# Kernel optimization log

Hardware: AMD Instinct MI355X
Metric: run time of the kernel (lower is better)

## Reference

```python
import jax, jax.numpy as jnp
import numpy as np

B, SQ, SK, D, H = 8, 2048, 2048, 512, 8
QP, KP, VP = 512, 512, 4096  # VP must equal D*H for O_w to accept the concat


def setup_inputs() -> dict:
    key = jax.random.key(0)
    ks = jax.random.split(key, 9)
    q_in = jax.random.normal(ks[0], (B, SQ, D), dtype=jnp.float32)
    k_in = jax.random.normal(ks[1], (B, SK, D), dtype=jnp.float32)
    v_in = jax.random.normal(ks[2], (B, SK, D), dtype=jnp.float32)
    mask = jax.random.randint(ks[3], (B, SQ, SK), 0, 2, dtype=jnp.int32)
    W_q = jax.random.normal(ks[4], (D, QP), dtype=jnp.float32) * 0.02
    W_k = jax.random.normal(ks[5], (D, KP), dtype=jnp.float32) * 0.02
    W_v = jax.random.normal(ks[6], (D, VP), dtype=jnp.float32) * 0.02
    W_o = jax.random.normal(ks[7], (VP, D), dtype=jnp.float32) * 0.02
    b_o = jnp.zeros((D,), dtype=jnp.float32)
    return {"q_in": q_in, "k_in": k_in, "v_in": v_in,
            "W_q": W_q, "W_k": W_k, "W_v": W_v, "W_o": W_o, "b_o": b_o,
            "mask": mask}


def reference(q_in, k_in, v_in, W_q, W_k, W_v, W_o, b_o, mask):
    b, sq, d = q_in.shape
    sk = k_in.shape[1]
    # NOTE: original scales by sqrt(input_dim // num_heads), NOT actual head dim
    scale = jnp.asarray(np.sqrt(d // H), dtype=q_in.dtype)
    q = q_in @ W_q  # (B, Sq, QP)
    k = k_in @ W_k  # (B, Sk, KP)
    v = v_in @ W_v  # (B, Sk, VP)
    q_h = q.reshape(b, sq, H, -1).transpose(0, 2, 1, 3)  # (B,H,Sq,dq)
    k_h = k.reshape(b, sk, H, -1).transpose(0, 2, 1, 3)  # (B,H,Sk,dk)
    v_h = v.reshape(b, sk, H, -1).transpose(0, 2, 1, 3)  # (B,H,Sk,dv)
    attn = jnp.einsum('bhid,bhkd->bhik', q_h, k_h)  # (B,H,Sq,Sk)
    attn = jnp.where(mask[:, None, :, :] == 0, jnp.asarray(-1e9, attn.dtype), attn)
    attn = jax.nn.softmax(attn / scale, axis=-1)
    out = attn @ v_h  # (B,H,Sq,dv)
    # Faithful to original bug: transpose(0,1) swaps BATCH and HEAD, then reshape
    out = jnp.transpose(out, (1, 0, 2, 3)).reshape(b, sq, -1)  # (B,Sq,H*dv)
    return out @ W_o + b_o
```

## Files before the change

### kernel.cpp

```cpp
#include <hip/hip_runtime.h>
#include <math.h>

typedef __bf16 bf16x8 __attribute__((ext_vector_type(8)));
typedef float fx4 __attribute__((ext_vector_type(4)));
typedef unsigned short u16;
typedef unsigned short u16x8 __attribute__((ext_vector_type(8)));
typedef unsigned int u32;
typedef unsigned char u8;

__device__ __forceinline__ fx4 mfma16(bf16x8 a, bf16x8 b, fx4 c) {
  return __builtin_amdgcn_mfma_f32_16x16x32_bf16(a, b, c, 0, 0, 0);
}
__device__ __forceinline__ u16 f2bf(float f) {
  u32 u = __float_as_uint(f);
  u += 0x7fffu + ((u >> 16) & 1u);
  return (u16)(u >> 16);
}
__device__ __forceinline__ float ex2(float x) { return __builtin_amdgcn_exp2f(x); }

#define BB 8
#define SS 2048
#define DD 512
#define HH 8
#define DQ 64
#define DV 512
#define VP 4096

#define OFF_QP  ((size_t)0)
#define OFF_KP  ((size_t)16777216)
#define OFF_WQT ((size_t)33554432)
#define OFF_WKT ((size_t)34078720)
#define OFF_WVT ((size_t)34603008)
#define OFF_WOT ((size_t)38797312)
#define OFF_MB  ((size_t)42991616)
#define OFF_VT  ((size_t)76546048)
#define OFF_XB  ((size_t)210763776)

__global__ __launch_bounds__(256) void transpose_w(const float* __restrict__ W,
                                                   u16* __restrict__ Wt,
                                                   int K, int N) {
  __shared__ float t[32][33];
  const int n0 = blockIdx.x * 32, k0 = blockIdx.y * 32;
  const int tx = threadIdx.x & 31, ty = threadIdx.x >> 5;
#pragma unroll
  for (int i = 0; i < 32; i += 8)
    t[ty + i][tx] = W[(size_t)(k0 + ty + i) * N + n0 + tx];
  __syncthreads();
#pragma unroll
  for (int i = 0; i < 32; i += 8)
    Wt[(size_t)(n0 + ty + i) * K + k0 + tx] = f2bf(t[tx][ty + i]);
}

__global__ __launch_bounds__(256) void mask_pack(const int* __restrict__ m,
                                                 u8* __restrict__ mb) {
  const size_t i = ((size_t)blockIdx.x * 256 + threadIdx.x) * 16;
  int4 a0 = *(const int4*)(m + i);
  int4 a1 = *(const int4*)(m + i + 4);
  int4 a2 = *(const int4*)(m + i + 8);
  int4 a3 = *(const int4*)(m + i + 12);
  uint4 o;
  o.x = (a0.x ? 1u : 0u) | ((a0.y ? 1u : 0u) << 8) | ((a0.z ? 1u : 0u) << 16) | ((a0.w ? 1u : 0u) << 24);
  o.y = (a1.x ? 1u : 0u) | ((a1.y ? 1u : 0u) << 8) | ((a1.z ? 1u : 0u) << 16) | ((a1.w ? 1u : 0u) << 24);
  o.z = (a2.x ? 1u : 0u) | ((a2.y ? 1u : 0u) << 8) | ((a2.z ? 1u : 0u) << 16) | ((a2.w ? 1u : 0u) << 24);
  o.w = (a3.x ? 1u : 0u) | ((a3.y ? 1u : 0u) << 8) | ((a3.z ? 1u : 0u) << 16) | ((a3.w ? 1u : 0u) << 24);
  *(uint4*)(mb + i) = o;
}

template <int AFP32, int EPI>
__global__ __launch_bounds__(256) void gemm_bt(const void* __restrict__ Ap,
                                               const u16* __restrict__ Bt,
                                               void* __restrict__ Cp,
                                               int M, int N, int K,
                                               const float* __restrict__ bias,
                                               float scale) {
  __shared__ union {
    struct { u16 As[128 * 32]; u16 Bs[128 * 32]; } s;
    u16 T[4][64 * 68];
  } sm;
  const int tid = threadIdx.x;
  const int lane = tid & 63, w = tid >> 6;
  const int lhi = lane >> 4, llo = lane & 15;
  const int wm = w >> 1, wn = w & 1;
  const int m0 = blockIdx.y * 128, n0 = blockIdx.x * 128;

  fx4 acc[4][4];
#pragma unroll
  for (int i = 0; i < 4; ++i)
#pragma unroll
    for (int j = 0; j < 4; ++j) acc[i][j] = (fx4){0.f, 0.f, 0.f, 0.f};

  for (int k0 = 0; k0 < K; k0 += 32) {
    if (AFP32) {
      const float* A = (const float*)Ap;
      const int row = tid >> 1, co = (tid & 1) * 16;
      const float* src = A + (size_t)(m0 + row) * K + k0 + co;
      float4 v0 = *(const float4*)(src + 0);
      float4 v1 = *(const float4*)(src + 4);
      float4 v2 = *(const float4*)(src + 8);
      float4 v3 = *(const float4*)(src + 12);
      u16x8 p0 = {f2bf(v0.x), f2bf(v0.y), f2bf(v0.z), f2bf(v0.w),
                  f2bf(v1.x), f2bf(v1.y), f2bf(v1.z), f2bf(v1.w)};
      u16x8 p1 = {f2bf(v2.x), f2bf(v2.y), f2bf(v2.z), f2bf(v2.w),
                  f2bf(v3.x), f2bf(v3.y), f2bf(v3.z), f2bf(v3.w)};
      *(u16x8*)&sm.s.As[row * 32 + co] = p0;
      *(u16x8*)&sm.s.As[row * 32 + co + 8] = p1;
    } else {
      const u16* A = (const u16*)Ap;
#pragma unroll
      for (int j = 0; j < 2; ++j) {
        int cc = j * 256 + tid;
        int row = cc >> 2, c8 = (cc & 3) * 8;
        *(uint4*)&sm.s.As[cc * 8] = *(const uint4*)&A[(size_t)(m0 + row) * K + k0 + c8];
      }
    }
#pragma unroll
    for (int j = 0; j < 2; ++j) {
      int cc = j * 256 + tid;
      int row = cc >> 2, c8 = (cc & 3) * 8;
      *(uint4*)&sm.s.Bs[cc * 8] = *(const uint4*)&Bt[(size_t)(n0 + row) * K + k0 + c8];
    }
    __syncthreads();
    bf16x8 af[4], bfv[4];
#pragma unroll
    for (int mi = 0; mi < 4; ++mi)
      af[mi] = *(const bf16x8*)&sm.s.As[(wm * 64 + mi * 16 + llo) * 32 + lhi * 8];
#pragma unroll
    for (int ni = 0; ni < 4; ++ni)
      bfv[ni] = *(const bf16x8*)&sm.s.Bs[(wn * 64 + ni * 16 + llo) * 32 + lhi * 8];
#pragma unroll
    for (int mi = 0; mi < 4; ++mi)
#pragma unroll
      for (int ni = 0; ni < 4; ++ni)
        acc[mi][ni] = mfma16(af[mi], bfv[ni], acc[mi][ni]);
    __syncthreads();
  }

  const int rbase = m0 + wm * 64, cbase = n0 + wn * 64;
  if (EPI == 0) {
    u16* C = (u16*)Cp;
#pragma unroll
    for (int mi = 0; mi < 4; ++mi) {
      int r0 = rbase + mi * 16 + lhi * 4;
#pragma unroll
      for (int ni = 0; ni < 4; ++ni) {
        int c = cbase + ni * 16 + llo;
#pragma unroll
        for (int r = 0; r < 4; ++r)
          C[(size_t)(r0 + r) * N + c] = f2bf(acc[mi][ni][r] * scale);
      }
    }
  } else if (EPI == 1) {
    u16* Tw = &sm.T[w][0];
#pragma unroll
    for (int mi = 0; mi < 4; ++mi)
#pragma unroll
      for (int ni = 0; ni < 4; ++ni) {
        ushort4 pk;
        pk.x = f2bf(acc[mi][ni][0]);
        pk.y = f2bf(acc[mi][ni][1]);
        pk.z = f2bf(acc[mi][ni][2]);
        pk.w = f2bf(acc[mi][ni][3]);
        *(ushort4*)&Tw[(ni * 16 + llo) * 68 + mi * 16 + lhi * 4] = pk;
      }
    u16* VtC = (u16*)Cp;
    const int bsel = rbase >> 11;
    const int sb = rbase & 2047;
    u16* dst = VtC + ((size_t)(bsel * VP + cbase + lane)) * SS + sb;
#pragma unroll
    for (int j = 0; j < 8; ++j) {
      u16x8 vv = *(u16x8*)&Tw[lane * 68 + j * 8];
      *(u16x8*)&dst[j * 8] = vv;
    }
  } else {
    float* C = (float*)Cp;
#pragma unroll
    for (int ni = 0; ni < 4; ++ni) {
      int c = cbase + ni * 16 + llo;
      float bv = bias[c];
#pragma unroll
      for (int mi = 0; mi < 4; ++mi) {
        int r0 = rbase + mi * 16 + lhi * 4;
#pragma unroll
        for (int r = 0; r < 4; ++r)
          C[(size_t)(r0 + r) * N + c] = acc[mi][ni][r] + bv;
      }
    }
  }
}

#define KB 128
#define SMS 132
__global__ __launch_bounds__(256, 2) void attn(const u16* __restrict__ Qp,
                                               const u16* __restrict__ Kp,
                                               const u16* __restrict__ Vt,
                                               const u8* __restrict__ mb,
                                               u16* __restrict__ Xb) {
  const int lin = blockIdx.x;
  const int xcd = lin & 7, idx = lin >> 3;
  const int chunk = idx >> 5, qt = idx & 31;
  const int b = chunk >> 1, dvh = chunk & 1, h = xcd;
  const int m0 = qt * 64;
  const int tid = threadIdx.x, w = tid >> 6, lane = tid & 63;
  const int lhi = lane >> 4, llo = lane & 15;

  __shared__ float Ssm[64 * SMS];
  __shared__ u16 Psm[64 * SMS];
  __shared__ float sm_l[64];

  bf16x8 qf[4][2];
#pragma unroll
  for (int mt = 0; mt < 4; ++mt)
#pragma unroll
    for (int ks = 0; ks < 2; ++ks)
      qf[mt][ks] = *(const bf16x8*)&Qp[(size_t)(b * SS + m0 + mt * 16 + llo) * 512 +
                                       h * DQ + ks * 32 + lhi * 8];

  fx4 acc[4][4];
#pragma unroll
  for (int mt = 0; mt < 4; ++mt)
#pragma unroll
    for (int nt = 0; nt < 4; ++nt) acc[mt][nt] = (fx4){0.f, 0.f, 0.f, 0.f};

  const int r8 = tid >> 3, c16 = (tid & 7) * 16;
  const u8* mr0 = mb + (size_t)(b * SS + m0 + r8) * SS;
  const u8* mr1 = mr0 + 32 * SS;
  float ls0 = 0.f, ls1 = 0.f;

  const int cw = w * 32;
  const size_t kbase = (size_t)(b * SS) * 512 + h * DQ + lhi * 8;
  const size_t vbase =
      (size_t)(b * VP + h * DV + dvh * 256 + w * 64 + llo) * SS + lhi * 8;

  for (int n0 = 0; n0 < SS; n0 += KB) {
    bf16x8 kf[2][2];
#pragma unroll
    for (int ct = 0; ct < 2; ++ct)
#pragma unroll
      for (int ks = 0; ks < 2; ++ks)
        kf[ct][ks] = *(const bf16x8*)&Kp[kbase +
                                         (size_t)(n0 + cw + ct * 16 + llo) * 512 +
                                         ks * 32];
    uint4 ma0 = *(const uint4*)&mr0[n0 + c16];
    uint4 ma1 = *(const uint4*)&mr1[n0 + c16];

#pragma unroll
    for (int ct = 0; ct < 2; ++ct)
#pragma unroll
      for (int mt = 0; mt < 4; ++mt) {
        fx4 s = (fx4){0.f, 0.f, 0.f, 0.f};
        s = mfma16(qf[mt][0], kf[ct][0], s);
        s = mfma16(qf[mt][1], kf[ct][1], s);
#pragma unroll
        for (int r = 0; r < 4; ++r)
          Ssm[(mt * 16 + lhi * 4 + r) * SMS + cw + ct * 16 + llo] = s[r];
      }
    __syncthreads();

#pragma unroll
    for (int half = 0; half < 2; ++half) {
      const int rr = r8 + half * 32;
      const uint4 mv = half ? ma1 : ma0;
      const float* Sr = &Ssm[rr * SMS + c16];
      float4 xa = *(const float4*)(Sr + 0);
      float4 xb = *(const float4*)(Sr + 4);
      float4 xc = *(const float4*)(Sr + 8);
      float4 xd = *(const float4*)(Sr + 12);
      const float NEG = -1.0e9f;
      float p0 = ex2((mv.x & 0x000000ffu) ? xa.x : NEG);
      float p1 = ex2((mv.x & 0x0000ff00u) ? xa.y : NEG);
      float p2 = ex2((mv.x & 0x00ff0000u) ? xa.z : NEG);
      float p3 = ex2((mv.x & 0xff000000u) ? xa.w : NEG);
      float p4 = ex2((mv.y & 0x000000ffu) ? xb.x : NEG);
      float p5 = ex2((mv.y & 0x0000ff00u) ? xb.y : NEG);
      float p6 = ex2((mv.y & 0x00ff0000u) ? xb.z : NEG);
      float p7 = ex2((mv.y & 0xff000000u) ? xb.w : NEG);
      float p8 = ex2((mv.z & 0x000000ffu) ? xc.x : NEG);
      float p9 = ex2((mv.z & 0x0000ff00u) ? xc.y : NEG);
      float p10 = ex2((mv.z & 0x00ff0000u) ? xc.z : NEG);
      float p11 = ex2((mv.z & 0xff000000u) ? xc.w : NEG);
      float p12 = ex2((mv.w & 0x000000ffu) ? xd.x : NEG);
      float p13 = ex2((mv.w & 0x0000ff00u) ? xd.y : NEG);
      float p14 = ex2((mv.w & 0x00ff0000u) ? xd.z : NEG);
      float p15 = ex2((mv.w & 0xff000000u) ? xd.w : NEG);
      u16x8 qa = {f2bf(p0), f2bf(p1), f2bf(p2), f2bf(p3),
                  f2bf(p4), f2bf(p5), f2bf(p6), f2bf(p7)};
      u16x8 qb = {f2bf(p8), f2bf(p9), f2bf(p10), f2bf(p11),
                  f2bf(p12), f2bf(p13), f2bf(p14), f2bf(p15)};
      *(u16x8*)&Psm[rr * SMS + c16] = qa;
      *(u16x8*)&Psm[rr * SMS + c16 + 8] = qb;
      float ps = (((p0 + p1) + (p2 + p3)) + ((p4 + p5) + (p6 + p7))) +
                 (((p8 + p9) + (p10 + p11)) + ((p12 + p13) + (p14 + p15)));
      if (half) ls1 += ps; else ls0 += ps;
    }
    __syncthreads();

#pragma unroll
    for (int kk = 0; kk < 4; ++kk) {
      bf16x8 pf[4];
#pragma unroll
      for (int mt = 0; mt < 4; ++mt)
        pf[mt] = *(const bf16x8*)&Psm[(mt * 16 + llo) * SMS + kk * 32 + lhi * 8];
      __builtin_amdgcn_s_setprio(1);
#pragma unroll
      for (int nt = 0; nt < 4; ++nt) {
        bf16x8 vf = *(const bf16x8*)&Vt[vbase + (size_t)(nt * 16) * SS + n0 + kk * 32];
#pragma unroll
        for (int mt = 0; mt < 4; ++mt)
          acc[mt][nt] = mfma16(pf[mt], vf, acc[mt][nt]);
      }
      __builtin_amdgcn_s_setprio(0);
    }
  }

  ls0 += __shfl_xor(ls0, 1); ls0 += __shfl_xor(ls0, 2); ls0 += __shfl_xor(ls0, 4);
  ls1 += __shfl_xor(ls1, 1); ls1 += __shfl_xor(ls1, 2); ls1 += __shfl_xor(ls1, 4);
  if ((tid & 7) == 0) { sm_l[r8] = ls0; sm_l[r8 + 32] = ls1; }
  __syncthreads();

  float linv[4][4];
#pragma unroll
  for (int mt = 0; mt < 4; ++mt)
#pragma unroll
    for (int r = 0; r < 4; ++r) linv[mt][r] = 1.0f / sm_l[mt * 16 + lhi * 4 + r];

  u16* Xs = (u16*)Ssm;
  const int er = tid >> 4, ec = (tid & 15) * 16;
#pragma unroll
  for (int mt = 0; mt < 4; ++mt) {
#pragma unroll
    for (int nt = 0; nt < 4; ++nt)
#pragma unroll
      for (int r = 0; r < 4; ++r)
        Xs[(lhi * 4 + r) * 264 + w * 64 + nt * 16 + llo] =
            f2bf(acc[mt][nt][r] * linv[mt][r]);
    __syncthreads();
    {
      const u16* src = Xs + er * 264 + ec;
      u16* dst = Xb + (size_t)((h * 8 + b) * SS + m0 + mt * 16 + er) * 512 +
                 dvh * 256 + ec;
      uint4 a0 = *(const uint4*)(src + 0);
      uint4 a1 = *(const uint4*)(src + 8);
      *(uint4*)(dst + 0) = a0;
      *(uint4*)(dst + 8) = a1;
    }
    __syncthreads();
  }
}

extern "C" void kernel_launch(void* const* d_in, const int* in_sizes, int n_in,
                              void* d_out, int out_size, void* d_ws, size_t ws_size,
                              hipStream_t stream) {
  (void)in_sizes; (void)n_in; (void)out_size; (void)ws_size;
  const float* q_in = (const float*)d_in[0];
  const float* k_in = (const float*)d_in[1];
  const float* v_in = (const float*)d_in[2];
  const float* W_q  = (const float*)d_in[3];
  const float* W_k  = (const float*)d_in[4];
  const float* W_v  = (const float*)d_in[5];
  const float* W_o  = (const float*)d_in[6];
  const float* b_o  = (const float*)d_in[7];
  const int*   mask = (const int*)d_in[8];

  char* ws = (char*)d_ws;
  u16* Qp   = (u16*)(ws + OFF_QP);
  u16* Kp   = (u16*)(ws + OFF_KP);
  u16* Wqt  = (u16*)(ws + OFF_WQT);
  u16* Wkt  = (u16*)(ws + OFF_WKT);
  u16* Wvt  = (u16*)(ws + OFF_WVT);
  u16* Wot  = (u16*)(ws + OFF_WOT);
  u8*  Mb   = (u8*)(ws + OFF_MB);
  u16* Vt   = (u16*)(ws + OFF_VT);
  u16* Xb   = (u16*)(ws + OFF_XB);

  transpose_w<<<dim3(16, 16), 256, 0, stream>>>(W_q, Wqt, 512, 512);
  transpose_w<<<dim3(16, 16), 256, 0, stream>>>(W_k, Wkt, 512, 512);
  transpose_w<<<dim3(128, 16), 256, 0, stream>>>(W_v, Wvt, 512, 4096);
  transpose_w<<<dim3(16, 128), 256, 0, stream>>>(W_o, Wot, 4096, 512);
  mask_pack<<<dim3(8192), 256, 0, stream>>>(mask, Mb);

  gemm_bt<1, 0><<<dim3(4, 128), 256, 0, stream>>>(q_in, Wqt, Qp, 16384, 512, 512, nullptr, 0.18033688011112f);
  gemm_bt<1, 0><<<dim3(4, 128), 256, 0, stream>>>(k_in, Wkt, Kp, 16384, 512, 512, nullptr, 1.0f);
  gemm_bt<1, 1><<<dim3(32, 128), 256, 0, stream>>>(v_in, Wvt, Vt, 16384, 4096, 512, nullptr, 1.0f);

  attn<<<dim3(4096), 256, 0, stream>>>(Qp, Kp, Vt, Mb, Xb);

  gemm_bt<0, 2><<<dim3(4, 128), 256, 0, stream>>>(Xb, Wot, d_out, 16384, 512, 4096, b_o, 1.0f);
}
```

Before: 1.392 ms.

## Fuse softmax into QK MFMA registers with swizzled double-buffered P tile

After: 1.492 ms (median of 2 runs). +7.2%, slower.

```diff
diff --git a/kernel.cpp b/kernel.cpp
--- a/kernel.cpp
+++ b/kernel.cpp
@@ -15,6 +15,10 @@
   u32 u = __float_as_uint(f);
   u += 0x7fffu + ((u >> 16) & 1u);
   return (u16)(u >> 16);
+}
+__device__ __forceinline__ u16 bfc(float f) {
+  __bf16 h = (__bf16)f;
+  return __builtin_bit_cast(u16, h);
 }
 __device__ __forceinline__ float ex2(float x) { return __builtin_amdgcn_exp2f(x); }
 
@@ -189,8 +193,7 @@
 }
 
 #define KB 128
-#define SMS 132
-__global__ __launch_bounds__(256, 2) void attn(const u16* __restrict__ Qp,
+__global__ __launch_bounds__(256, 3) void attn(const u16* __restrict__ Qp,
                                                const u16* __restrict__ Kp,
                                                const u16* __restrict__ Vt,
                                                const u8* __restrict__ mb,
@@ -202,9 +205,10 @@
   const int m0 = qt * 64;
   const int tid = threadIdx.x, w = tid >> 6, lane = tid & 63;
   const int lhi = lane >> 4, llo = lane & 15;
-
-  __shared__ float Ssm[64 * SMS];
-  __shared__ u16 Psm[64 * SMS];
+  const int xork = (llo & 7) << 4;
+
+  __shared__ u16 Psm[2][64 * 128];
+  __shared__ float sm_lw[4][64];
   __shared__ float sm_l[64];
 
   bf16x8 qf[4][2];
@@ -220,77 +224,53 @@
   for (int mt = 0; mt < 4; ++mt)
 #pragma unroll
     for (int nt = 0; nt < 4; ++nt) acc[mt][nt] = (fx4){0.f, 0.f, 0.f, 0.f};
-
-  const int r8 = tid >> 3, c16 = (tid & 7) * 16;
-  const u8* mr0 = mb + (size_t)(b * SS + m0 + r8) * SS;
-  const u8* mr1 = mr0 + 32 * SS;
-  float ls0 = 0.f, ls1 = 0.f;
-
-  const int cw = w * 32;
+  float lp[4] = {0.f, 0.f, 0.f, 0.f};
+
   const size_t kbase = (size_t)(b * SS) * 512 + h * DQ + lhi * 8;
   const size_t vbase =
       (size_t)(b * VP + h * DV + dvh * 256 + w * 64 + llo) * SS + lhi * 8;
+  const u8* mrow[4];
+#pragma unroll
+  for (int mt = 0; mt < 4; ++mt)
+    mrow[mt] = mb + (size_t)(b * SS + m0 + mt * 16 + llo) * SS + w * 32 + lhi * 4;
 
   for (int n0 = 0; n0 < SS; n0 += KB) {
+    const int buf = (n0 >> 7) & 1;
+    char* Pb = (char*)&Psm[buf][0];
+
     bf16x8 kf[2][2];
 #pragma unroll
-    for (int ct = 0; ct < 2; ++ct)
+    for (int st = 0; st < 2; ++st)
 #pragma unroll
       for (int ks = 0; ks < 2; ++ks)
-        kf[ct][ks] = *(const bf16x8*)&Kp[kbase +
-                                         (size_t)(n0 + cw + ct * 16 + llo) * 512 +
+        kf[st][ks] = *(const bf16x8*)&Kp[kbase +
+                                         (size_t)(n0 + w * 32 + st * 16 + llo) * 512 +
                                          ks * 32];
-    uint4 ma0 = *(const uint4*)&mr0[n0 + c16];
-    uint4 ma1 = *(const uint4*)&mr1[n0 + c16];
-
-#pragma unroll
-    for (int ct = 0; ct < 2; ++ct)
-#pragma unroll
-      for (int mt = 0; mt < 4; ++mt) {
+    u32 mv[4][2];
+#pragma unroll
+    for (int mt = 0; mt < 4; ++mt)
+#pragma unroll
+      for (int st = 0; st < 2; ++st)
+        mv[mt][st] = *(const u32*)(mrow[mt] + n0 + st * 16);
+
+#pragma unroll
+    for (int mt = 0; mt < 4; ++mt) {
+      const int qL = mt * 16 + llo;
+      char* prow = Pb + qL * 256;
+#pragma unroll
+      for (int st = 0; st < 2; ++st) {
         fx4 s = (fx4){0.f, 0.f, 0.f, 0.f};
-        s = mfma16(qf[mt][0], kf[ct][0], s);
-        s = mfma16(qf[mt][1], kf[ct][1], s);
-#pragma unroll
-        for (int r = 0; r < 4; ++r)
-          Ssm[(mt * 16 + lhi * 4 + r) * SMS + cw + ct * 16 + llo] = s[r];
-      }
-    __syncthreads();
-
-#pragma unroll
-    for (int half = 0; half < 2; ++half) {
-      const int rr = r8 + half * 32;
-      const uint4 mv = half ? ma1 : ma0;
-      const float* Sr = &Ssm[rr * SMS + c16];
-      float4 xa = *(const float4*)(Sr + 0);
-      float4 xb = *(const float4*)(Sr + 4);
-      float4 xc = *(const float4*)(Sr + 8);
-      float4 xd = *(const float4*)(Sr + 12);
-      const float NEG = -1.0e9f;
-      float p0 = ex2((mv.x & 0x000000ffu) ? xa.x : NEG);
-      float p1 = ex2((mv.x & 0x0000ff00u) ? xa.y : NEG);
-      float p2 = ex2((mv.x & 0x00ff0000u) ? xa.z : NEG);
-      float p3 = ex2((mv.x & 0xff000000u) ? xa.w : NEG);
-      float p4 = ex2((mv.y & 0x000000ffu) ? xb.x : NEG);
-      float p5 = ex2((mv.y & 0x0000ff00u) ? xb.y : NEG);
-      float p6 = ex2((mv.y & 0x00ff0000u) ? xb.z : NEG);
-      float p7 = ex2((mv.y & 0xff000000u) ? xb.w : NEG);
-      float p8 = ex2((mv.z & 0x000000ffu) ? xc.x : NEG);
-      float p9 = ex2((mv.z & 0x0000ff00u) ? xc.y : NEG);
-      float p10 = ex2((mv.z & 0x00ff0000u) ? xc.z : NEG);
-      float p11 = ex2((mv.z & 0xff000000u) ? xc.w : NEG);
-      float p12 = ex2((mv.w & 0x000000ffu) ? xd.x : NEG);
-      float p13 = ex2((mv.w & 0x0000ff00u) ? xd.y : NEG);
-      float p14 = ex2((mv.w & 0x00ff0000u) ? xd.z : NEG);
-      float p15 = ex2((mv.w & 0xff000000u) ? xd.w : NEG);
-      u16x8 qa = {f2bf(p0), f2bf(p1), f2bf(p2), f2bf(p3),
-                  f2bf(p4), f2bf(p5), f2bf(p6), f2bf(p7)};
-      u16x8 qb = {f2bf(p8), f2bf(p9), f2bf(p10), f2bf(p11),
-                  f2bf(p12), f2bf(p13), f2bf(p14), f2bf(p15)};
-      *(u16x8*)&Psm[rr * SMS + c16] = qa;
-      *(u16x8*)&Psm[rr * SMS + c16 + 8] = qb;
-      float ps = (((p0 + p1) + (p2 + p3)) + ((p4 + p5) + (p6 + p7))) +
-                 (((p8 + p9) + (p10 + p11)) + ((p12 + p13) + (p14 + p15)));
-      if (half) ls1 += ps; else ls0 += ps;
+        s = mfma16(kf[st][0], qf[mt][0], s);
+        s = mfma16(kf[st][1], qf[mt][1], s);
+        const u32 m = mv[mt][st];
+        float p0 = (m & 0x000000ffu) ? ex2(s[0]) : 0.f;
+        float p1 = (m & 0x0000ff00u) ? ex2(s[1]) : 0.f;
+        float p2 = (m & 0x00ff0000u) ? ex2(s[2]) : 0.f;
+        float p3 = (m & 0xff000000u) ? ex2(s[3]) : 0.f;
+        lp[mt] += (p0 + p1) + (p2 + p3);
+        ushort4 pk = {bfc(p0), bfc(p1), bfc(p2), bfc(p3)};
+        *(ushort4*)(prow + ((w * 64 + st * 32 + lhi * 8) ^ xork)) = pk;
+      }
     }
     __syncthreads();
 
@@ -299,7 +279,8 @@
       bf16x8 pf[4];
 #pragma unroll
       for (int mt = 0; mt < 4; ++mt)
-        pf[mt] = *(const bf16x8*)&Psm[(mt * 16 + llo) * SMS + kk * 32 + lhi * 8];
+        pf[mt] = *(const bf16x8*)(Pb + (mt * 16 + llo) * 256 +
+                                  ((kk * 64 + lhi * 16) ^ xork));
       __builtin_amdgcn_s_setprio(1);
 #pragma unroll
       for (int nt = 0; nt < 4; ++nt) {
@@ -312,10 +293,19 @@
     }
   }
 
-  ls0 += __shfl_xor(ls0, 1); ls0 += __shfl_xor(ls0, 2); ls0 += __shfl_xor(ls0, 4);
-  ls1 += __shfl_xor(ls1, 1); ls1 += __shfl_xor(ls1, 2); ls1 += __shfl_xor(ls1, 4);
-  if ((tid & 7) == 0) { sm_l[r8] = ls0; sm_l[r8 + 32] = ls1; }
+#pragma unroll
+  for (int mt = 0; mt < 4; ++mt) {
+    lp[mt] += __shfl_xor(lp[mt], 16);
+    lp[mt] += __shfl_xor(lp[mt], 32);
+  }
+  if (lhi == 0) {
+#pragma unroll
+    for (int mt = 0; mt < 4; ++mt) sm_lw[w][mt * 16 + llo] = lp[mt];
+  }
   __syncthreads();
+  if (tid < 64)
+    sm_l[tid] = (sm_lw[0][tid] + sm_lw[1][tid]) + (sm_lw[2][tid] + sm_lw[3][tid]);
+  __syncthreads();
 
   float linv[4][4];
 #pragma unroll
@@ -323,7 +313,7 @@
 #pragma unroll
     for (int r = 0; r < 4; ++r) linv[mt][r] = 1.0f / sm_l[mt * 16 + lhi * 4 + r];
 
-  u16* Xs = (u16*)Ssm;
+  u16* Xs = (u16*)&Psm[0][0];
   const int er = tid >> 4, ec = (tid & 15) * 16;
 #pragma unroll
   for (int mt = 0; mt < 4; ++mt) {
```
